# Optimization experiments

Hardware: AMD Instinct MI355X
Metric: run time of the kernel (lower is better)

Reference implementation:

```python
import jax, jax.numpy as jnp
import numpy as np
from jax import lax

B, T, I, H, O = 256, 128, 512, 1024, 512


def setup_inputs() -> dict:
    key = jax.random.key(0)
    ks = jax.random.split(key, 7)
    s = 1.0 / np.sqrt(H)  # PyTorch LSTM/Linear init bound
    x = jax.random.normal(ks[0], (B, T, I), dtype=jnp.float32)
    W_ih = jax.random.uniform(ks[1], (4 * H, I), jnp.float32, -s, s)
    W_hh = jax.random.uniform(ks[2], (4 * H, H), jnp.float32, -s, s)
    b_ih = jax.random.uniform(ks[3], (4 * H,), jnp.float32, -s, s)
    b_hh = jax.random.uniform(ks[4], (4 * H,), jnp.float32, -s, s)
    W_fc = jax.random.uniform(ks[5], (O, H), jnp.float32, -s, s)
    b_fc = jax.random.uniform(ks[6], (O,), jnp.float32, -s, s)
    return {"x": x, "W_ih": W_ih, "W_hh": W_hh, "b_ih": b_ih,
            "b_hh": b_hh, "W_fc": W_fc, "b_fc": b_fc}


def _lstm_last(x, W_ih, W_hh, b_ih, b_hh):
    # Precompute input contribution for all timesteps: [T, B, 4H]
    pre = jnp.einsum('bti,gi->tbg', x, W_ih) + b_ih + b_hh

    def step(carry, xg):
        h, c = carry
        gates = xg + h @ W_hh.T  # [B, 4H]
        i, f, g, o = jnp.split(gates, 4, axis=-1)  # PyTorch gate order i,f,g,o
        c = jax.nn.sigmoid(f) * c + jax.nn.sigmoid(i) * jnp.tanh(g)
        h = jax.nn.sigmoid(o) * jnp.tanh(c)
        return (h, c), None

    h0 = jnp.zeros((x.shape[0], W_hh.shape[1]), x.dtype)
    (h, c), _ = lax.scan(step, (h0, h0), pre)
    return h, c


def reference(x, W_ih, W_hh, b_ih, b_hh, W_fc, b_fc):
    h, c = _lstm_last(x, W_ih, W_hh, b_ih, b_hh)
    out = h @ W_fc.T + b_fc  # fc on last timestep hidden
    # hidden returned as (h_n, c_n) with leading n_layers=1 dim, as in PyTorch
    return out, (h[None], c[None])
```

## Files before the change

### kernel.cpp

```cpp
#include <hip/hip_runtime.h>

typedef short bf8 __attribute__((ext_vector_type(8)));
typedef float f32x4 __attribute__((ext_vector_type(4)));

static constexpr int BB = 256;
static constexpr int TT = 128;
static constexpr int II = 512;
static constexpr int HH = 1024;
static constexpr int OO = 512;
static constexpr int G4 = 4096;

static constexpr size_t OUT_H = (size_t)BB * OO;
static constexpr size_t OUT_C = OUT_H + (size_t)BB * HH;
static constexpr size_t HBUF  = (size_t)BB * HH;

__device__ __forceinline__ float bf2f(ushort u) {
    unsigned v = ((unsigned)u) << 16;
    return __builtin_bit_cast(float, v);
}
__device__ __forceinline__ ushort f2bf(float f) {
    unsigned x = __builtin_bit_cast(unsigned, f);
    x = x + 0x7FFFu + ((x >> 16) & 1u);
    return (ushort)(x >> 16);
}
__device__ __forceinline__ float sigf(float x) { return 1.0f / (1.0f + __expf(-x)); }
__device__ __forceinline__ float tanhf_(float x) { return 2.0f * sigf(2.0f * x) - 1.0f; }

__device__ __forceinline__ void st_wt_short(const ushort* p, uint v) {
    asm volatile("global_store_short %0, %1, off sc0 sc1" :: "v"(p), "v"(v) : "memory");
}
__device__ __forceinline__ void st_wt_b64(const ushort* p, uint2 v) {
    asm volatile("global_store_dwordx2 %0, %1, off sc0 sc1" :: "v"(p), "v"(v) : "memory");
}
__device__ __forceinline__ void ld_bp_ushort_issue(uint& dst, const ushort* p) {
    asm volatile("global_load_ushort %0, %1, off sc0 sc1" : "=v"(dst) : "v"(p) : "memory");
}
__device__ __forceinline__ void ld_bp_b128_issue(uint4& dst, const ushort* p) {
    asm volatile("global_load_dwordx4 %0, %1, off sc0 sc1" : "=v"(dst) : "v"(p) : "memory");
}
__device__ __forceinline__ void wait_vm0() {
    asm volatile("s_waitcnt vmcnt(0)" ::: "memory");
    __builtin_amdgcn_sched_barrier(0);
}

__device__ __forceinline__ void lightbar(int* slots, int bg, int gen) {
    asm volatile("s_waitcnt vmcnt(0) lgkmcnt(0)" ::: "memory");
    __builtin_amdgcn_sched_barrier(0);
    __syncthreads();
    int tid = threadIdx.x;
    if (tid == 0) {
        asm volatile("global_store_dword %0, %1, off sc0 sc1" :: "v"(slots + bg * 32), "v"(gen) : "memory");
    }
    if (tid < 64) {
        const int* sp = slots + tid * 32;
        int v;
        do {
            asm volatile("global_load_dword %0, %1, off sc0 sc1\n\ts_waitcnt vmcnt(0)"
                         : "=v"(v) : "v"(sp) : "memory");
            if (v >= gen) break;
            __builtin_amdgcn_s_sleep(1);
        } while (true);
    }
    __syncthreads();
}

__global__ void k_init(int* slots) {
    int i = blockIdx.x * 256 + threadIdx.x;
    if (i < 4 * 64 * 32) slots[i] = 0;
}

__global__ void k_cast(const float* __restrict__ src, ushort* __restrict__ dst, int n4) {
    int i = blockIdx.x * blockDim.x + threadIdx.x;
    int stride = gridDim.x * blockDim.x;
    for (; i < n4; i += stride) {
        float4 v = ((const float4*)src)[i];
        ushort4 o;
        o.x = f2bf(v.x); o.y = f2bf(v.y); o.z = f2bf(v.z); o.w = f2bf(v.w);
        ((ushort4*)dst)[i] = o;
    }
}

__global__ void k_prep_w(const float* __restrict__ w, ushort* __restrict__ wp,
                         const float* __restrict__ bi, const float* __restrict__ bh,
                         float* __restrict__ bp, int Kdim) {
    int p = blockIdx.x;
    int orig = ((p >> 4) & 3) * HH + ((p >> 6) << 4) + (p & 15);
    const float* src = w + (size_t)orig * Kdim;
    ushort* dst = wp + (size_t)p * Kdim;
    for (int k = threadIdx.x; k < Kdim; k += 256) dst[k] = f2bf(src[k]);
    if (threadIdx.x == 0 && bp) bp[p] = bi[orig] + bh[orig];
}

__global__ __launch_bounds__(256) void k_main(
    const float* __restrict__ x, const ushort* __restrict__ wpih,
    const float* __restrict__ bp, ushort* __restrict__ pre,
    const ushort* __restrict__ wphh, ushort* __restrict__ hbf,
    float* __restrict__ dout, int* slots_all, int SEG) {
    __shared__ ushort wl[32 * 2048];
    __shared__ ushort Al[64 * 32];
    __shared__ ushort Bl[128 * 32];

    int tid = threadIdx.x;
    int bid = blockIdx.x;
    int g  = bid >> 6;
    int bg = bid & 63;
    int j  = bg;
    int row0 = g << 6;
    int* slots = slots_all + g * 64 * 32;
    int gen = 0;

    {
        const ushort* wsrc = wphh + (size_t)(j << 6) * HH;
        for (int s = 0; s < 32; ++s) {
            int cidx = (s << 8) + tid;
            int c = cidx >> 7;
            int kc = cidx & 127;
            uint4 v = *(const uint4*)(wsrc + (size_t)c * HH + (kc << 3));
            int byte = ((kc >> 2) << 12) + ((((c << 6) + ((kc & 3) << 4))) ^ ((c & 7) << 4));
            *(uint4*)((char*)wl + byte) = v;
        }
        int r = tid >> 2, hc = (tid & 3) << 2;
        uint2 z; z.x = 0; z.y = 0;
        st_wt_b64(hbf + (size_t)(row0 + r) * HH + (j << 4) + hc, z);
    }

    int w = tid >> 6, l = tid & 63;
    int wm = w >> 1, wn = w & 1;
    int l15 = l & 15, kg = l >> 4;
    int swz = (l15 & 7) << 4;
    int wbase = ((l15 << 6) + (kg << 4)) ^ swz;

    int r0 = tid >> 2, kk = tid & 3;
    int sbyteA = ((r0 << 6) + (kk << 4)) ^ ((r0 & 7) << 4);
    int sbyteB1 = sbyteA + 4096;

    const ushort* hrow0 = hbf + (size_t)(row0 + (w << 4) + l15) * HH + (kg << 3);
    int drow = row0 + (w << 4) + (kg << 2);
    int hcol = (j << 4) + l15;
    ushort* hout0 = hbf + (size_t)drow * HH + hcol;
    const ushort* pbase = pre + (size_t)drow * G4 + (j << 6) + l15;
    float creg[4] = {0.f, 0.f, 0.f, 0.f};

    int nseg = TT / SEG;
    for (int sg = 0; sg < nseg; ++sg) {
        int t0 = sg * SEG;
        int ntiles = SEG << 5;
        for (int q = bg; q < ntiles; q += 64) {
            int trel = q >> 5;
            int t = t0 + trel;
            int n0 = (q & 31) << 7;
            const float* xa = x + ((size_t)(row0 + r0) * TT + t) * II + (kk << 3);
            const ushort* gb0 = wpih + (size_t)(n0 + r0) * II + (kk << 3);
            const ushort* gb1 = gb0 + (size_t)64 * II;
            f32x4 acc[2][4];
#pragma unroll
            for (int mi = 0; mi < 2; ++mi)
#pragma unroll
                for (int ni = 0; ni < 4; ++ni) acc[mi][ni] = f32x4{0.f, 0.f, 0.f, 0.f};
            float4 a0 = *(const float4*)xa;
            float4 a1 = *(const float4*)(xa + 4);
            uint4 b0v = *(const uint4*)gb0;
            uint4 b1v = *(const uint4*)gb1;
            for (int ko = 0; ko < 16; ++ko) {
                union { ushort us[8]; uint4 v; } pa;
                pa.us[0] = f2bf(a0.x); pa.us[1] = f2bf(a0.y); pa.us[2] = f2bf(a0.z); pa.us[3] = f2bf(a0.w);
                pa.us[4] = f2bf(a1.x); pa.us[5] = f2bf(a1.y); pa.us[6] = f2bf(a1.z); pa.us[7] = f2bf(a1.w);
                __syncthreads();
                *(uint4*)((char*)Al + sbyteA) = pa.v;
                *(uint4*)((char*)Bl + sbyteA) = b0v;
                *(uint4*)((char*)Bl + sbyteB1) = b1v;
                __syncthreads();
                if (ko < 15) {
                    int k = (ko + 1) << 5;
                    a0 = *(const float4*)(xa + k);
                    a1 = *(const float4*)(xa + k + 4);
                    b0v = *(const uint4*)(gb0 + k);
                    b1v = *(const uint4*)(gb1 + k);
                }
                bf8 af[2], bv[4];
#pragma unroll
                for (int mi = 0; mi < 2; ++mi)
                    af[mi] = *(const bf8*)((char*)Al + wm * 2048 + mi * 1024 + wbase);
#pragma unroll
                for (int ni = 0; ni < 4; ++ni)
                    bv[ni] = *(const bf8*)((char*)Bl + wn * 4096 + ni * 1024 + wbase);
#pragma unroll
                for (int mi = 0; mi < 2; ++mi)
#pragma unroll
                    for (int ni = 0; ni < 4; ++ni)
                        acc[mi][ni] = __builtin_amdgcn_mfma_f32_16x16x32_bf16(af[mi], bv[ni], acc[mi][ni], 0, 0, 0);
            }
#pragma unroll
            for (int ni = 0; ni < 4; ++ni) {
                int col = n0 + wn * 64 + ni * 16 + l15;
                float bias = bp[col];
#pragma unroll
                for (int mi = 0; mi < 2; ++mi) {
                    int arow = row0 + wm * 32 + mi * 16 + (kg << 2);
#pragma unroll
                    for (int r = 0; r < 4; ++r) {
                        const ushort* pp = pre + ((size_t)trel * BB + arow + r) * G4 + col;
                        st_wt_short(pp, (uint)f2bf(acc[mi][ni][r] + bias));
                    }
                }
            }
        }
        gen++; lightbar(slots, bg, gen);

        uint prn[16];
#pragma unroll
        for (int ni = 0; ni < 4; ++ni)
#pragma unroll
            for (int r = 0; r < 4; ++r)
                ld_bp_ushort_issue(prn[ni * 4 + r], pbase + (size_t)r * G4 + ni * 16);

        for (int trel = 0; trel < SEG; ++trel) {
            int t = t0 + trel;
            wait_vm0();
            f32x4 acc[4];
#pragma unroll
            for (int ni = 0; ni < 4; ++ni)
#pragma unroll
                for (int r = 0; r < 4; ++r) acc[ni][r] = bf2f((ushort)prn[ni * 4 + r]);

            const ushort* hr = hrow0 + (size_t)(t & 1) * HBUF;
#pragma unroll
            for (int c = 0; c < 4; ++c) {
                uint4 hv[8];
#pragma unroll
                for (int u = 0; u < 8; ++u)
                    ld_bp_b128_issue(hv[u], hr + ((c * 8 + u) << 5));
                wait_vm0();
#pragma unroll
                for (int u = 0; u < 8; ++u) {
                    int ko = c * 8 + u;
                    bf8 a = __builtin_bit_cast(bf8, hv[u]);
#pragma unroll
                    for (int ni = 0; ni < 4; ++ni) {
                        bf8 b = *(const bf8*)((char*)wl + ko * 4096 + ni * 1024 + wbase);
                        acc[ni] = __builtin_amdgcn_mfma_f32_16x16x32_bf16(a, b, acc[ni], 0, 0, 0);
                    }
                }
            }

            if (trel < SEG - 1) {
                const ushort* pn = pbase + (size_t)(trel + 1) * ((size_t)BB * G4);
#pragma unroll
                for (int ni = 0; ni < 4; ++ni)
#pragma unroll
                    for (int r = 0; r < 4; ++r)
                        ld_bp_ushort_issue(prn[ni * 4 + r], pn + (size_t)r * G4 + ni * 16);
            }

            ushort* ho = hout0 + (size_t)((t & 1) ^ 1) * HBUF;
            bool last = (t == TT - 1);
#pragma unroll
            for (int r = 0; r < 4; ++r) {
                float ig = sigf(acc[0][r]);
                float fg = sigf(acc[1][r]);
                float gg = tanhf_(acc[2][r]);
                float og = sigf(acc[3][r]);
                float c = fg * creg[r] + ig * gg;
                creg[r] = c;
                float h = og * tanhf_(c);
                st_wt_short(ho + (size_t)r * HH, (uint)f2bf(h));
                if (last) {
                    dout[OUT_H + (size_t)(drow + r) * HH + hcol] = h;
                    dout[OUT_C + (size_t)(drow + r) * HH + hcol] = c;
                }
            }
            gen++; lightbar(slots, bg, gen);
        }
    }
}

__global__ __launch_bounds__(256) void k_fc(const ushort* __restrict__ hbf,
                                            const ushort* __restrict__ wfc,
                                            const float* __restrict__ bfc,
                                            float* __restrict__ out) {
    int tid = threadIdx.x;
    int b0 = (blockIdx.x >> 3) << 6;
    int n0 = (blockIdx.x & 7) << 6;
    int w = tid >> 6, l = tid & 63;
    int l15 = l & 15, kg = l >> 4;
    const ushort* ha = hbf + (size_t)(b0 + (w << 4) + l15) * HH + (kg << 3);
    f32x4 acc[4];
#pragma unroll
    for (int ni = 0; ni < 4; ++ni) acc[ni] = f32x4{0.f, 0.f, 0.f, 0.f};
    for (int ko = 0; ko < 32; ++ko) {
        bf8 a = *(const bf8*)(ha + (ko << 5));
#pragma unroll
        for (int ni = 0; ni < 4; ++ni) {
            bf8 b = *(const bf8*)(wfc + (size_t)(n0 + ni * 16 + l15) * HH + (ko << 5) + (kg << 3));
            acc[ni] = __builtin_amdgcn_mfma_f32_16x16x32_bf16(a, b, acc[ni], 0, 0, 0);
        }
    }
    int drow = b0 + (w << 4) + (kg << 2);
#pragma unroll
    for (int ni = 0; ni < 4; ++ni) {
        int col = n0 + ni * 16 + l15;
        float bias = bfc[col];
#pragma unroll
        for (int r = 0; r < 4; ++r)
            out[(size_t)(drow + r) * OO + col] = acc[ni][r] + bias;
    }
}

extern "C" void kernel_launch(void* const* d_in, const int* in_sizes, int n_in,
                              void* d_out, int out_size, void* d_ws, size_t ws_size,
                              hipStream_t stream) {
    const float* x   = (const float*)d_in[0];
    const float* Wih = (const float*)d_in[1];
    const float* Whh = (const float*)d_in[2];
    const float* bih = (const float*)d_in[3];
    const float* bhh = (const float*)d_in[4];
    const float* Wfc = (const float*)d_in[5];
    const float* bfc = (const float*)d_in[6];
    float* out = (float*)d_out;

    char* ws = (char*)d_ws;
    size_t off = 0;
    ushort* wpih = (ushort*)(ws + off); off += (size_t)G4 * II * 2;
    ushort* wphh = (ushort*)(ws + off); off += (size_t)G4 * HH * 2;
    ushort* wfcb = (ushort*)(ws + off); off += (size_t)OO * HH * 2;
    float*  bp   = (float*)(ws + off);  off += (size_t)G4 * 4;
    ushort* hbf  = (ushort*)(ws + off); off += (size_t)2 * BB * HH * 2;
    int*    slots= (int*)(ws + off);    off += (size_t)4 * 64 * 32 * 4;
    size_t fixed = off;
    int SEG = 16;
    while (SEG > 1 && fixed + (size_t)SEG * BB * G4 * 2 > ws_size) SEG >>= 1;
    ushort* pre = (ushort*)(ws + off);

    k_init<<<32, 256, 0, stream>>>(slots);
    k_cast<<<256, 256, 0, stream>>>(Wfc, wfcb, OO * HH / 4);
    k_prep_w<<<G4, 256, 0, stream>>>(Wih, wpih, bih, bhh, bp, II);
    k_prep_w<<<G4, 256, 0, stream>>>(Whh, wphh, nullptr, nullptr, nullptr, HH);
    k_main<<<256, 256, 0, stream>>>(x, wpih, bp, pre, wphh, hbf, out, slots, SEG);
    k_fc<<<32, 256, 0, stream>>>(hbf, wfcb, bfc, out);
}
```

Before: 1.649 ms.

## Split LSTM kernel into producer and consumer blocks with a ring-buffered input projection

Splits the persistent kernel into 128 producer blocks, which compute the input projection into a two-slot ring of segment buffers, and 128 consumer blocks that run the recurrence. The two sides hand off through seg_done and seg_used counters. Each consumer now covers 128 batch rows (two M tiles per wave) and double-buffers its h loads with partial vmcnt waits. The aim is to overlap the input GEMM with the serial recurrence and remove the per-segment barrier across all blocks. The cost is that only half the blocks run the recurrence, so each does twice the MFMA work per step, and producer-to-consumer polling adds latency.

```diff
diff --git a/kernel.cpp b/kernel.cpp
--- a/kernel.cpp
+++ b/kernel.cpp
@@ -2,6 +2,7 @@
 
 typedef short bf8 __attribute__((ext_vector_type(8)));
 typedef float f32x4 __attribute__((ext_vector_type(4)));
+typedef uint u32x4 __attribute__((ext_vector_type(4)));
 
 static constexpr int BB = 256;
 static constexpr int TT = 128;
@@ -9,6 +10,9 @@
 static constexpr int HH = 1024;
 static constexpr int OO = 512;
 static constexpr int G4 = 4096;
+static constexpr int NCONS = 128;
+static constexpr int NPROD = 128;
+static constexpr int RING = 2;
 
 static constexpr size_t OUT_H = (size_t)BB * OO;
 static constexpr size_t OUT_C = OUT_H + (size_t)BB * HH;
@@ -29,18 +33,32 @@
 __device__ __forceinline__ void st_wt_short(const ushort* p, uint v) {
     asm volatile("global_store_short %0, %1, off sc0 sc1" :: "v"(p), "v"(v) : "memory");
 }
-__device__ __forceinline__ void st_wt_b64(const ushort* p, uint2 v) {
-    asm volatile("global_store_dwordx2 %0, %1, off sc0 sc1" :: "v"(p), "v"(v) : "memory");
+__device__ __forceinline__ void st_wt_b128(const ushort* p, u32x4 v) {
+    asm volatile("global_store_dwordx4 %0, %1, off sc0 sc1" :: "v"(p), "v"(v) : "memory");
 }
 __device__ __forceinline__ void ld_bp_ushort_issue(uint& dst, const ushort* p) {
     asm volatile("global_load_ushort %0, %1, off sc0 sc1" : "=v"(dst) : "v"(p) : "memory");
 }
-__device__ __forceinline__ void ld_bp_b128_issue(uint4& dst, const ushort* p) {
+__device__ __forceinline__ void ld_bp_b128_issue(u32x4& dst, const ushort* p) {
     asm volatile("global_load_dwordx4 %0, %1, off sc0 sc1" : "=v"(dst) : "v"(p) : "memory");
 }
 __device__ __forceinline__ void wait_vm0() {
     asm volatile("s_waitcnt vmcnt(0)" ::: "memory");
     __builtin_amdgcn_sched_barrier(0);
+}
+#define WAITVM(N) do { asm volatile("s_waitcnt vmcnt(" #N ")" ::: "memory"); \
+                       __builtin_amdgcn_sched_barrier(0); } while (0)
+
+template <int SLP>
+__device__ __forceinline__ int poll_ge(const int* p, int target) {
+    int v;
+    do {
+        asm volatile("global_load_dword %0, %1, off sc0 sc1\n\ts_waitcnt vmcnt(0)"
+                     : "=v"(v) : "v"(p) : "memory");
+        if (v >= target) break;
+        __builtin_amdgcn_s_sleep(SLP);
+    } while (true);
+    return v;
 }
 
 __device__ __forceinline__ void lightbar(int* slots, int bg, int gen) {
@@ -48,9 +66,8 @@
     __builtin_amdgcn_sched_barrier(0);
     __syncthreads();
     int tid = threadIdx.x;
-    if (tid == 0) {
+    if (tid == 0)
         asm volatile("global_store_dword %0, %1, off sc0 sc1" :: "v"(slots + bg * 32), "v"(gen) : "memory");
-    }
     if (tid < 64) {
         const int* sp = slots + tid * 32;
         int v;
@@ -64,9 +81,9 @@
     __syncthreads();
 }
 
-__global__ void k_init(int* slots) {
+__global__ void k_init(int* flags) {
     int i = blockIdx.x * 256 + threadIdx.x;
-    if (i < 4 * 64 * 32) slots[i] = 0;
+    if (i < 4608) flags[i] = 0;
 }
 
 __global__ void k_cast(const float* __restrict__ src, ushort* __restrict__ dst, int n4) {
@@ -95,18 +112,105 @@
     const float* __restrict__ x, const ushort* __restrict__ wpih,
     const float* __restrict__ bp, ushort* __restrict__ pre,
     const ushort* __restrict__ wphh, ushort* __restrict__ hbf,
-    float* __restrict__ dout, int* slots_all, int SEG) {
+    float* __restrict__ dout, int* flags, int SEG) {
     __shared__ ushort wl[32 * 2048];
     __shared__ ushort Al[64 * 32];
     __shared__ ushort Bl[128 * 32];
 
     int tid = threadIdx.x;
     int bid = blockIdx.x;
-    int g  = bid >> 6;
-    int bg = bid & 63;
-    int j  = bg;
-    int row0 = g << 6;
-    int* slots = slots_all + g * 64 * 32;
+    int* seg_done = flags + 4096;
+    int* seg_used = flags + 4224;
+    int nseg = TT / SEG;
+    size_t SEGEL = (size_t)SEG * BB * G4;
+
+    int w = tid >> 6, l = tid & 63;
+    int l15 = l & 15, kg = l >> 4;
+    int wbase = ((l15 << 6) + (kg << 4)) ^ ((l15 & 7) << 4);
+
+    if (bid >= NCONS) {
+        int pid = bid - NCONS;
+        int wm = w >> 1, wn = w & 1;
+        int r0 = tid >> 2, kk = tid & 3;
+        int sbyteA = ((r0 << 6) + (kk << 4)) ^ ((r0 & 7) << 4);
+        int sbyteB1 = sbyteA + 4096;
+        for (int sg = 0; sg < nseg; ++sg) {
+            if (sg >= RING) {
+                if (tid == 0) poll_ge<8>(seg_used + sg - RING, NCONS);
+                __syncthreads();
+            }
+            ushort* sb = pre + (size_t)(sg % RING) * SEGEL;
+            for (int i = 0; i < SEG; ++i) {
+                int q = pid + (i << 7);
+                int tm = q >> 5, tn = q & 31;
+                int trel = tm >> 2, b0 = (tm & 3) << 6, n0 = tn << 7;
+                int t = sg * SEG + trel;
+                const float* xa = x + ((size_t)(b0 + r0) * TT + t) * II + (kk << 3);
+                const ushort* gb0 = wpih + (size_t)(n0 + r0) * II + (kk << 3);
+                const ushort* gb1 = gb0 + (size_t)64 * II;
+                f32x4 acc[2][4];
+#pragma unroll
+                for (int mi = 0; mi < 2; ++mi)
+#pragma unroll
+                    for (int ni = 0; ni < 4; ++ni) acc[mi][ni] = f32x4{0.f, 0.f, 0.f, 0.f};
+                float4 a0 = *(const float4*)xa;
+                float4 a1 = *(const float4*)(xa + 4);
+                uint4 b0v = *(const uint4*)gb0;
+                uint4 b1v = *(const uint4*)gb1;
+                for (int ko = 0; ko < 16; ++ko) {
+                    union { ushort us[8]; uint4 v; } pa;
+                    pa.us[0] = f2bf(a0.x); pa.us[1] = f2bf(a0.y); pa.us[2] = f2bf(a0.z); pa.us[3] = f2bf(a0.w);
+                    pa.us[4] = f2bf(a1.x); pa.us[5] = f2bf(a1.y); pa.us[6] = f2bf(a1.z); pa.us[7] = f2bf(a1.w);
+                    __syncthreads();
+                    *(uint4*)((char*)Al + sbyteA) = pa.v;
+                    *(uint4*)((char*)Bl + sbyteA) = b0v;
+                    *(uint4*)((char*)Bl + sbyteB1) = b1v;
+                    __syncthreads();
+                    if (ko < 15) {
+                        int k = (ko + 1) << 5;
+                        a0 = *(const float4*)(xa + k);
+                        a1 = *(const float4*)(xa + k + 4);
+                        b0v = *(const uint4*)(gb0 + k);
+                        b1v = *(const uint4*)(gb1 + k);
+                    }
+                    bf8 af[2], bv[4];
+#pragma unroll
+                    for (int mi = 0; mi < 2; ++mi)
+                        af[mi] = *(const bf8*)((char*)Al + wm * 2048 + mi * 1024 + wbase);
+#pragma unroll
+                    for (int ni = 0; ni < 4; ++ni)
+                        bv[ni] = *(const bf8*)((char*)Bl + wn * 4096 + ni * 1024 + wbase);
+#pragma unroll
+                    for (int mi = 0; mi < 2; ++mi)
+#pragma unroll
+                        for (int ni = 0; ni < 4; ++ni)
+                            acc[mi][ni] = __builtin_amdgcn_mfma_f32_16x16x32_bf16(af[mi], bv[ni], acc[mi][ni], 0, 0, 0);
+                }
+#pragma unroll
+                for (int ni = 0; ni < 4; ++ni) {
+                    int col = n0 + wn * 64 + ni * 16 + l15;
+                    float bias = bp[col];
+#pragma unroll
+                    for (int mi = 0; mi < 2; ++mi) {
+                        int arow = b0 + wm * 32 + mi * 16 + (kg << 2);
+#pragma unroll
+                        for (int r = 0; r < 4; ++r)
+                            st_wt_short(sb + ((size_t)trel * BB + arow + r) * G4 + col,
+                                        (uint)f2bf(acc[mi][ni][r] + bias));
+                    }
+                }
+            }
+            asm volatile("s_waitcnt vmcnt(0)" ::: "memory");
+            __builtin_amdgcn_sched_barrier(0);
+            __syncthreads();
+            if (tid == 0) atomicAdd(seg_done + sg, 1);
+        }
+        return;
+    }
+
+    int g = bid >> 6, j = bid & 63;
+    int row0 = g << 7;
+    int* slots = flags + g * 2048;
     int gen = 0;
 
     {
@@ -119,157 +223,137 @@
             int byte = ((kc >> 2) << 12) + ((((c << 6) + ((kc & 3) << 4))) ^ ((c & 7) << 4));
             *(uint4*)((char*)wl + byte) = v;
         }
-        int r = tid >> 2, hc = (tid & 3) << 2;
-        uint2 z; z.x = 0; z.y = 0;
-        st_wt_b64(hbf + (size_t)(row0 + r) * HH + (j << 4) + hc, z);
-    }
-
-    int w = tid >> 6, l = tid & 63;
-    int wm = w >> 1, wn = w & 1;
-    int l15 = l & 15, kg = l >> 4;
-    int swz = (l15 & 7) << 4;
-    int wbase = ((l15 << 6) + (kg << 4)) ^ swz;
-
-    int r0 = tid >> 2, kk = tid & 3;
-    int sbyteA = ((r0 << 6) + (kk << 4)) ^ ((r0 & 7) << 4);
-    int sbyteB1 = sbyteA + 4096;
-
-    const ushort* hrow0 = hbf + (size_t)(row0 + (w << 4) + l15) * HH + (kg << 3);
-    int drow = row0 + (w << 4) + (kg << 2);
+        int r = tid >> 1, hc = (tid & 1) << 3;
+        u32x4 z = {0, 0, 0, 0};
+        st_wt_b128(hbf + (size_t)(row0 + r) * HH + (j << 4) + hc, z);
+    }
+
+    int rw = row0 + (w << 5);
+    const ushort* hA0 = hbf + (size_t)(rw + l15) * HH + (kg << 3);
+    const ushort* hA1 = hbf + (size_t)(rw + 16 + l15) * HH + (kg << 3);
+    int dr0 = rw + (kg << 2);
+    int dr1 = rw + 16 + (kg << 2);
     int hcol = (j << 4) + l15;
-    ushort* hout0 = hbf + (size_t)drow * HH + hcol;
-    const ushort* pbase = pre + (size_t)drow * G4 + (j << 6) + l15;
-    float creg[4] = {0.f, 0.f, 0.f, 0.f};
-
-    int nseg = TT / SEG;
+    ushort* ho0 = hbf + (size_t)dr0 * HH + hcol;
+    ushort* ho1 = hbf + (size_t)dr1 * HH + hcol;
+    float creg[8] = {0.f, 0.f, 0.f, 0.f, 0.f, 0.f, 0.f, 0.f};
+
+    gen++; lightbar(slots, j, gen);
+
+    uint prn[32];
     for (int sg = 0; sg < nseg; ++sg) {
-        int t0 = sg * SEG;
-        int ntiles = SEG << 5;
-        for (int q = bg; q < ntiles; q += 64) {
-            int trel = q >> 5;
-            int t = t0 + trel;
-            int n0 = (q & 31) << 7;
-            const float* xa = x + ((size_t)(row0 + r0) * TT + t) * II + (kk << 3);
-            const ushort* gb0 = wpih + (size_t)(n0 + r0) * II + (kk << 3);
-            const ushort* gb1 = gb0 + (size_t)64 * II;
-            f32x4 acc[2][4];
-#pragma unroll
-            for (int mi = 0; mi < 2; ++mi)
-#pragma unroll
-                for (int ni = 0; ni < 4; ++ni) acc[mi][ni] = f32x4{0.f, 0.f, 0.f, 0.f};
-            float4 a0 = *(const float4*)xa;
-            float4 a1 = *(const float4*)(xa + 4);
-            uint4 b0v = *(const uint4*)gb0;
-            uint4 b1v = *(const uint4*)gb1;
-            for (int ko = 0; ko < 16; ++ko) {
-                union { ushort us[8]; uint4 v; } pa;
-                pa.us[0] = f2bf(a0.x); pa.us[1] = f2bf(a0.y); pa.us[2] = f2bf(a0.z); pa.us[3] = f2bf(a0.w);
-                pa.us[4] = f2bf(a1.x); pa.us[5] = f2bf(a1.y); pa.us[6] = f2bf(a1.z); pa.us[7] = f2bf(a1.w);
-                __syncthreads();
-                *(uint4*)((char*)Al + sbyteA) = pa.v;
-                *(uint4*)((char*)Bl + sbyteA) = b0v;
-                *(uint4*)((char*)Bl + sbyteB1) = b1v;
-                __syncthreads();
-                if (ko < 15) {
-                    int k = (ko + 1) << 5;
-                    a0 = *(const float4*)(xa + k);
-                    a1 = *(const float4*)(xa + k + 4);
-                    b0v = *(const uint4*)(gb0 + k);
-                    b1v = *(const uint4*)(gb1 + k);
-                }
-                bf8 af[2], bv[4];
-#pragma unroll
-                for (int mi = 0; mi < 2; ++mi)
-                    af[mi] = *(const bf8*)((char*)Al + wm * 2048 + mi * 1024 + wbase);
+        ushort* sb = pre + (size_t)(sg % RING) * SEGEL;
+        if (sg > 0 && tid == 0) atomicAdd(seg_used + sg - 1, 1);
+        if (tid == 0) poll_ge<2>(seg_done + sg, NPROD);
+        __syncthreads();
+        {
+            const ushort* pn0 = sb + (size_t)dr0 * G4 + (j << 6) + l15;
+            const ushort* pn1 = sb + (size_t)dr1 * G4 + (j << 6) + l15;
+#pragma unroll
+            for (int ni = 0; ni < 4; ++ni)
+#pragma unroll
+                for (int r = 0; r < 4; ++r) {
+                    ld_bp_ushort_issue(prn[ni * 4 + r], pn0 + (size_t)r * G4 + (ni << 4));
+                    ld_bp_ushort_issue(prn[16 + ni * 4 + r], pn1 + (size_t)r * G4 + (ni << 4));
+                }
+            wait_vm0();
+        }
+
+        for (int trel = 0; trel < SEG; ++trel) {
+            int t = sg * SEG + trel;
+            const ushort* hr0 = hA0 + (size_t)(t & 1) * HBUF;
+            const ushort* hr1 = hA1 + (size_t)(t & 1) * HBUF;
+            u32x4 x0[8], x1[8], y0[8], y1[8];
+
+#define ISSUE8(B0, B1, C) \
+            _Pragma("unroll") \
+            for (int u = 0; u < 8; ++u) { \
+                ld_bp_b128_issue(B0[u], hr0 + (((C) * 8 + u) << 5)); \
+                ld_bp_b128_issue(B1[u], hr1 + (((C) * 8 + u) << 5)); \
+            }
+#define CONSUME8(B0, B1, C) \
+            _Pragma("unroll") \
+            for (int u = 0; u < 8; ++u) { \
+                int ko = (C) * 8 + u; \
+                bf8 a0 = __builtin_bit_cast(bf8, B0[u]); \
+                bf8 a1 = __builtin_bit_cast(bf8, B1[u]); \
+                _Pragma("unroll") \
+                for (int ni = 0; ni < 4; ++ni) { \
+                    bf8 b = *(const bf8*)((char*)wl + ko * 4096 + ni * 1024 + wbase); \
+                    acc0[ni] = __builtin_amdgcn_mfma_f32_16x16x32_bf16(a0, b, acc0[ni], 0, 0, 0); \
+                    acc1[ni] = __builtin_amdgcn_mfma_f32_16x16x32_bf16(a1, b, acc1[ni], 0, 0, 0); \
+                } \
+            }
+
+            f32x4 acc0[4], acc1[4];
+            ISSUE8(x0, x1, 0)
+            ISSUE8(y0, y1, 1)
+#pragma unroll
+            for (int ni = 0; ni < 4; ++ni)
+#pragma unroll
+                for (int r = 0; r < 4; ++r) {
+                    acc0[ni][r] = bf2f((ushort)prn[ni * 4 + r]);
+                    acc1[ni][r] = bf2f((ushort)prn[16 + ni * 4 + r]);
+                }
+            WAITVM(16);
+            CONSUME8(x0, x1, 0)
+            ISSUE8(x0, x1, 2)
+            WAITVM(16);
+            CONSUME8(y0, y1, 1)
+            ISSUE8(y0, y1, 3)
+            WAITVM(16);
+            CONSUME8(x0, x1, 2)
+            {
+                int nrel = (trel + 1 < SEG) ? trel + 1 : 0;
+                const ushort* pn0 = sb + ((size_t)nrel * BB + dr0) * G4 + (j << 6) + l15;
+                const ushort* pn1 = sb + ((size_t)nrel * BB + dr1) * G4 + (j << 6) + l15;
 #pragma unroll
                 for (int ni = 0; ni < 4; ++ni)
-                    bv[ni] = *(const bf8*)((char*)Bl + wn * 4096 + ni * 1024 + wbase);
-#pragma unroll
-                for (int mi = 0; mi < 2; ++mi)
-#pragma unroll
-                    for (int ni = 0; ni < 4; ++ni)
-                        acc[mi][ni] = __builtin_amdgcn_mfma_f32_16x16x32_bf16(af[mi], bv[ni], acc[mi][ni], 0, 0, 0);
-            }
-#pragma unroll
-            for (int ni = 0; ni < 4; ++ni) {
-                int col = n0 + wn * 64 + ni * 16 + l15;
-                float bias = bp[col];
-#pragma unroll
-                for (int mi = 0; mi < 2; ++mi) {
-                    int arow = row0 + wm * 32 + mi * 16 + (kg << 2);
 #pragma unroll
                     for (int r = 0; r < 4; ++r) {
-                        const ushort* pp = pre + ((size_t)trel * BB + arow + r) * G4 + col;
-                        st_wt_short(pp, (uint)f2bf(acc[mi][ni][r] + bias));
+                        ld_bp_ushort_issue(prn[ni * 4 + r], pn0 + (size_t)r * G4 + (ni << 4));
+                        ld_bp_ushort_issue(prn[16 + ni * 4 + r], pn1 + (size_t)r * G4 + (ni << 4));
                     }
-                }
-            }
-        }
-        gen++; lightbar(slots, bg, gen);
-
-        uint prn[16];
-#pragma unroll
-        for (int ni = 0; ni < 4; ++ni)
-#pragma unroll
-            for (int r = 0; r < 4; ++r)
-                ld_bp_ushort_issue(prn[ni * 4 + r], pbase + (size_t)r * G4 + ni * 16);
-
-        for (int trel = 0; trel < SEG; ++trel) {
-            int t = t0 + trel;
-            wait_vm0();
-            f32x4 acc[4];
-#pragma unroll
-            for (int ni = 0; ni < 4; ++ni)
-#pragma unroll
-                for (int r = 0; r < 4; ++r) acc[ni][r] = bf2f((ushort)prn[ni * 4 + r]);
-
-            const ushort* hr = hrow0 + (size_t)(t & 1) * HBUF;
-#pragma unroll
-            for (int c = 0; c < 4; ++c) {
-                uint4 hv[8];
-#pragma unroll
-                for (int u = 0; u < 8; ++u)
-                    ld_bp_b128_issue(hv[u], hr + ((c * 8 + u) << 5));
-                wait_vm0();
-#pragma unroll
-                for (int u = 0; u < 8; ++u) {
-                    int ko = c * 8 + u;
-                    bf8 a = __builtin_bit_cast(bf8, hv[u]);
-#pragma unroll
-                    for (int ni = 0; ni < 4; ++ni) {
-                        bf8 b = *(const bf8*)((char*)wl + ko * 4096 + ni * 1024 + wbase);
-                        acc[ni] = __builtin_amdgcn_mfma_f32_16x16x32_bf16(a, b, acc[ni], 0, 0, 0);
-                    }
-                }
-            }
-
-            if (trel < SEG - 1) {
-                const ushort* pn = pbase + (size_t)(trel + 1) * ((size_t)BB * G4);
-#pragma unroll
-                for (int ni = 0; ni < 4; ++ni)
-#pragma unroll
-                    for (int r = 0; r < 4; ++r)
-                        ld_bp_ushort_issue(prn[ni * 4 + r], pn + (size_t)r * G4 + ni * 16);
-            }
-
-            ushort* ho = hout0 + (size_t)((t & 1) ^ 1) * HBUF;
+            }
+            WAITVM(32);
+            CONSUME8(y0, y1, 3)
+#undef ISSUE8
+#undef CONSUME8
+
+            ushort* h0 = ho0 + (size_t)((t & 1) ^ 1) * HBUF;
+            ushort* h1 = ho1 + (size_t)((t & 1) ^ 1) * HBUF;
             bool last = (t == TT - 1);
 #pragma unroll
             for (int r = 0; r < 4; ++r) {
-                float ig = sigf(acc[0][r]);
-                float fg = sigf(acc[1][r]);
-                float gg = tanhf_(acc[2][r]);
-                float og = sigf(acc[3][r]);
+                float ig = sigf(acc0[0][r]);
+                float fg = sigf(acc0[1][r]);
+                float gg = tanhf_(acc0[2][r]);
+                float og = sigf(acc0[3][r]);
                 float c = fg * creg[r] + ig * gg;
                 creg[r] = c;
                 float h = og * tanhf_(c);
-                st_wt_short(ho + (size_t)r * HH, (uint)f2bf(h));
+                st_wt_short(h0 + (size_t)r * HH, (uint)f2bf(h));
                 if (last) {
-                    dout[OUT_H + (size_t)(drow + r) * HH + hcol] = h;
-                    dout[OUT_C + (size_t)(drow + r) * HH + hcol] = c;
-                }
-            }
-            gen++; lightbar(slots, bg, gen);
+                    dout[OUT_H + (size_t)(dr0 + r) * HH + hcol] = h;
+                    dout[OUT_C + (size_t)(dr0 + r) * HH + hcol] = c;
+                }
+            }
+#pragma unroll
+            for (int r = 0; r < 4; ++r) {
+                float ig = sigf(acc1[0][r]);
+                float fg = sigf(acc1[1][r]);
+                float gg = tanhf_(acc1[2][r]);
+                float og = sigf(acc1[3][r]);
+                float c = fg * creg[4 + r] + ig * gg;
+                creg[4 + r] = c;
+                float h = og * tanhf_(c);
+                st_wt_short(h1 + (size_t)r * HH, (uint)f2bf(h));
+                if (last) {
+                    dout[OUT_H + (size_t)(dr1 + r) * HH + hcol] = h;
+                    dout[OUT_C + (size_t)(dr1 + r) * HH + hcol] = c;
+                }
+            }
+            gen++; lightbar(slots, j, gen);
         }
     }
 }
@@ -325,16 +409,16 @@
     ushort* wfcb = (ushort*)(ws + off); off += (size_t)OO * HH * 2;
     float*  bp   = (float*)(ws + off);  off += (size_t)G4 * 4;
     ushort* hbf  = (ushort*)(ws + off); off += (size_t)2 * BB * HH * 2;
-    int*    slots= (int*)(ws + off);    off += (size_t)4 * 64 * 32 * 4;
+    int*    flags= (int*)(ws + off);    off += 4608 * 4;
     size_t fixed = off;
     int SEG = 16;
-    while (SEG > 1 && fixed + (size_t)SEG * BB * G4 * 2 > ws_size) SEG >>= 1;
+    while (SEG > 1 && fixed + (size_t)RING * SEG * BB * G4 * 2 > ws_size) SEG >>= 1;
     ushort* pre = (ushort*)(ws + off);
 
-    k_init<<<32, 256, 0, stream>>>(slots);
+    k_init<<<18, 256, 0, stream>>>(flags);
     k_cast<<<256, 256, 0, stream>>>(Wfc, wfcb, OO * HH / 4);
     k_prep_w<<<G4, 256, 0, stream>>>(Wih, wpih, bih, bhh, bp, II);
     k_prep_w<<<G4, 256, 0, stream>>>(Whh, wphh, nullptr, nullptr, nullptr, HH);
-    k_main<<<256, 256, 0, stream>>>(x, wpih, bp, pre, wphh, hbf, out, slots, SEG);
+    k_main<<<256, 256, 0, stream>>>(x, wpih, bp, pre, wphh, hbf, out, flags, SEG);
     k_fc<<<32, 256, 0, stream>>>(hbf, wfcb, bfc, out);
 }
```

After: 1.791 ms. 8.7% more time.

## Use per-timestep h buffers with cached loads and software-pipeline h fetches

Applied to the files above, without the earlier changes.

When the workspace allows, the hidden state is written to a separate buffer for each timestep (T+1 buffers) rather than a ping-pong pair. Because an address is never rewritten, the recurrent h loads can use ordinary cached global loads instead of cache-bypassing ones. The h-fetch loop is also double-buffered: two groups of 8 dwordx4 loads stay in flight with partial vmcnt waits, and the next step's preactivation loads are issued during compute instead of after it. The cost is a much larger workspace footprint, which can shrink SEG, and correctness now depends on cache coherence across blocks for never-reused addresses.

```diff
diff --git a/kernel.cpp b/kernel.cpp
--- a/kernel.cpp
+++ b/kernel.cpp
@@ -2,6 +2,7 @@
 
 typedef short bf8 __attribute__((ext_vector_type(8)));
 typedef float f32x4 __attribute__((ext_vector_type(4)));
+typedef uint u32x4 __attribute__((ext_vector_type(4)));
 
 static constexpr int BB = 256;
 static constexpr int TT = 128;
@@ -35,22 +36,26 @@
 __device__ __forceinline__ void ld_bp_ushort_issue(uint& dst, const ushort* p) {
     asm volatile("global_load_ushort %0, %1, off sc0 sc1" : "=v"(dst) : "v"(p) : "memory");
 }
-__device__ __forceinline__ void ld_bp_b128_issue(uint4& dst, const ushort* p) {
+__device__ __forceinline__ void ld_bp_b128_issue(u32x4& dst, const ushort* p) {
     asm volatile("global_load_dwordx4 %0, %1, off sc0 sc1" : "=v"(dst) : "v"(p) : "memory");
+}
+__device__ __forceinline__ void ld_c_b128_issue(u32x4& dst, const ushort* p) {
+    asm volatile("global_load_dwordx4 %0, %1, off" : "=v"(dst) : "v"(p) : "memory");
 }
 __device__ __forceinline__ void wait_vm0() {
     asm volatile("s_waitcnt vmcnt(0)" ::: "memory");
     __builtin_amdgcn_sched_barrier(0);
 }
+#define WAITVM(N) do { asm volatile("s_waitcnt vmcnt(" #N ")" ::: "memory"); \
+                       __builtin_amdgcn_sched_barrier(0); } while (0)
 
 __device__ __forceinline__ void lightbar(int* slots, int bg, int gen) {
     asm volatile("s_waitcnt vmcnt(0) lgkmcnt(0)" ::: "memory");
     __builtin_amdgcn_sched_barrier(0);
     __syncthreads();
     int tid = threadIdx.x;
-    if (tid == 0) {
+    if (tid == 0)
         asm volatile("global_store_dword %0, %1, off sc0 sc1" :: "v"(slots + bg * 32), "v"(gen) : "memory");
-    }
     if (tid < 64) {
         const int* sp = slots + tid * 32;
         int v;
@@ -64,9 +69,9 @@
     __syncthreads();
 }
 
-__global__ void k_init(int* slots) {
+__global__ void k_init(int* flags) {
     int i = blockIdx.x * 256 + threadIdx.x;
-    if (i < 4 * 64 * 32) slots[i] = 0;
+    if (i < 8192) flags[i] = 0;
 }
 
 __global__ void k_cast(const float* __restrict__ src, ushort* __restrict__ dst, int n4) {
@@ -91,23 +96,27 @@
     if (threadIdx.x == 0 && bp) bp[p] = bi[orig] + bh[orig];
 }
 
+template <int HMODE>
 __global__ __launch_bounds__(256) void k_main(
     const float* __restrict__ x, const ushort* __restrict__ wpih,
     const float* __restrict__ bp, ushort* __restrict__ pre,
     const ushort* __restrict__ wphh, ushort* __restrict__ hbf,
-    float* __restrict__ dout, int* slots_all, int SEG) {
+    float* __restrict__ dout, int* flags, int SEG) {
     __shared__ ushort wl[32 * 2048];
     __shared__ ushort Al[64 * 32];
     __shared__ ushort Bl[128 * 32];
 
     int tid = threadIdx.x;
     int bid = blockIdx.x;
-    int g  = bid >> 6;
-    int bg = bid & 63;
-    int j  = bg;
+    int g = bid >> 6, j = bid & 63;
     int row0 = g << 6;
-    int* slots = slots_all + g * 64 * 32;
+    int* slots = flags + g * 2048;
     int gen = 0;
+    int nseg = TT / SEG;
+
+    int w = tid >> 6, l = tid & 63;
+    int l15 = l & 15, kg = l >> 4;
+    int wbase = ((l15 << 6) + (kg << 4)) ^ ((l15 & 7) << 4);
 
     {
         const ushort* wsrc = wphh + (size_t)(j << 6) * HH;
@@ -124,28 +133,22 @@
         st_wt_b64(hbf + (size_t)(row0 + r) * HH + (j << 4) + hc, z);
     }
 
-    int w = tid >> 6, l = tid & 63;
     int wm = w >> 1, wn = w & 1;
-    int l15 = l & 15, kg = l >> 4;
-    int swz = (l15 & 7) << 4;
-    int wbase = ((l15 << 6) + (kg << 4)) ^ swz;
-
     int r0 = tid >> 2, kk = tid & 3;
     int sbyteA = ((r0 << 6) + (kk << 4)) ^ ((r0 & 7) << 4);
     int sbyteB1 = sbyteA + 4096;
 
-    const ushort* hrow0 = hbf + (size_t)(row0 + (w << 4) + l15) * HH + (kg << 3);
+    const ushort* hbase = hbf + (size_t)(row0 + (w << 4) + l15) * HH + (kg << 3);
     int drow = row0 + (w << 4) + (kg << 2);
     int hcol = (j << 4) + l15;
-    ushort* hout0 = hbf + (size_t)drow * HH + hcol;
+    ushort* hobase = hbf + (size_t)drow * HH + hcol;
     const ushort* pbase = pre + (size_t)drow * G4 + (j << 6) + l15;
     float creg[4] = {0.f, 0.f, 0.f, 0.f};
 
-    int nseg = TT / SEG;
     for (int sg = 0; sg < nseg; ++sg) {
         int t0 = sg * SEG;
         int ntiles = SEG << 5;
-        for (int q = bg; q < ntiles; q += 64) {
+        for (int q = j; q < ntiles; q += 64) {
             int trel = q >> 5;
             int t = t0 + trel;
             int n0 = (q & 31) << 7;
@@ -198,61 +201,77 @@
                 for (int mi = 0; mi < 2; ++mi) {
                     int arow = row0 + wm * 32 + mi * 16 + (kg << 2);
 #pragma unroll
-                    for (int r = 0; r < 4; ++r) {
-                        const ushort* pp = pre + ((size_t)trel * BB + arow + r) * G4 + col;
-                        st_wt_short(pp, (uint)f2bf(acc[mi][ni][r] + bias));
-                    }
+                    for (int r = 0; r < 4; ++r)
+                        st_wt_short(pre + ((size_t)trel * BB + arow + r) * G4 + col,
+                                    (uint)f2bf(acc[mi][ni][r] + bias));
                 }
             }
         }
-        gen++; lightbar(slots, bg, gen);
+        gen++; lightbar(slots, j, gen);
 
         uint prn[16];
 #pragma unroll
         for (int ni = 0; ni < 4; ++ni)
 #pragma unroll
             for (int r = 0; r < 4; ++r)
-                ld_bp_ushort_issue(prn[ni * 4 + r], pbase + (size_t)r * G4 + ni * 16);
+                ld_bp_ushort_issue(prn[ni * 4 + r], pbase + (size_t)r * G4 + (ni << 4));
+        wait_vm0();
 
         for (int trel = 0; trel < SEG; ++trel) {
             int t = t0 + trel;
-            wait_vm0();
+            int rb = HMODE ? (t & 1) : t;
+            int wb = HMODE ? ((t & 1) ^ 1) : (t + 1);
+            const ushort* hr = hbase + (size_t)rb * HBUF;
+            u32x4 xv[8], yv[8];
+
+#define ISSUE8(B, C) \
+            _Pragma("unroll") \
+            for (int u = 0; u < 8; ++u) { \
+                if constexpr (HMODE == 0) ld_c_b128_issue(B[u], hr + (((C) * 8 + u) << 5)); \
+                else ld_bp_b128_issue(B[u], hr + (((C) * 8 + u) << 5)); \
+            }
+#define CONSUME8(B, C) \
+            _Pragma("unroll") \
+            for (int u = 0; u < 8; ++u) { \
+                int ko = (C) * 8 + u; \
+                bf8 a = __builtin_bit_cast(bf8, B[u]); \
+                _Pragma("unroll") \
+                for (int ni = 0; ni < 4; ++ni) { \
+                    bf8 b = *(const bf8*)((char*)wl + ko * 4096 + ni * 1024 + wbase); \
+                    acc[ni] = __builtin_amdgcn_mfma_f32_16x16x32_bf16(a, b, acc[ni], 0, 0, 0); \
+                } \
+            }
+
             f32x4 acc[4];
+            ISSUE8(xv, 0)
+            ISSUE8(yv, 1)
 #pragma unroll
             for (int ni = 0; ni < 4; ++ni)
 #pragma unroll
                 for (int r = 0; r < 4; ++r) acc[ni][r] = bf2f((ushort)prn[ni * 4 + r]);
-
-            const ushort* hr = hrow0 + (size_t)(t & 1) * HBUF;
-#pragma unroll
-            for (int c = 0; c < 4; ++c) {
-                uint4 hv[8];
-#pragma unroll
-                for (int u = 0; u < 8; ++u)
-                    ld_bp_b128_issue(hv[u], hr + ((c * 8 + u) << 5));
-                wait_vm0();
-#pragma unroll
-                for (int u = 0; u < 8; ++u) {
-                    int ko = c * 8 + u;
-                    bf8 a = __builtin_bit_cast(bf8, hv[u]);
-#pragma unroll
-                    for (int ni = 0; ni < 4; ++ni) {
-                        bf8 b = *(const bf8*)((char*)wl + ko * 4096 + ni * 1024 + wbase);
-                        acc[ni] = __builtin_amdgcn_mfma_f32_16x16x32_bf16(a, b, acc[ni], 0, 0, 0);
-                    }
-                }
-            }
-
-            if (trel < SEG - 1) {
-                const ushort* pn = pbase + (size_t)(trel + 1) * ((size_t)BB * G4);
+            WAITVM(8);
+            CONSUME8(xv, 0)
+            ISSUE8(xv, 2)
+            WAITVM(8);
+            CONSUME8(yv, 1)
+            ISSUE8(yv, 3)
+            WAITVM(8);
+            CONSUME8(xv, 2)
+            {
+                int nrel = (trel + 1 < SEG) ? trel + 1 : 0;
+                const ushort* pnn = pre + ((size_t)nrel * BB + drow) * G4 + (j << 6) + l15;
 #pragma unroll
                 for (int ni = 0; ni < 4; ++ni)
 #pragma unroll
                     for (int r = 0; r < 4; ++r)
-                        ld_bp_ushort_issue(prn[ni * 4 + r], pn + (size_t)r * G4 + ni * 16);
-            }
-
-            ushort* ho = hout0 + (size_t)((t & 1) ^ 1) * HBUF;
+                        ld_bp_ushort_issue(prn[ni * 4 + r], pnn + (size_t)r * G4 + (ni << 4));
+            }
+            WAITVM(16);
+            CONSUME8(yv, 3)
+#undef ISSUE8
+#undef CONSUME8
+
+            ushort* ho = hobase + (size_t)wb * HBUF;
             bool last = (t == TT - 1);
 #pragma unroll
             for (int r = 0; r < 4; ++r) {
@@ -269,12 +288,12 @@
                     dout[OUT_C + (size_t)(drow + r) * HH + hcol] = c;
                 }
             }
-            gen++; lightbar(slots, bg, gen);
+            gen++; lightbar(slots, j, gen);
         }
     }
 }
 
-__global__ __launch_bounds__(256) void k_fc(const ushort* __restrict__ hbf,
+__global__ __launch_bounds__(256) void k_fc(const ushort* __restrict__ hlast,
                                             const ushort* __restrict__ wfc,
                                             const float* __restrict__ bfc,
                                             float* __restrict__ out) {
@@ -283,7 +302,7 @@
     int n0 = (blockIdx.x & 7) << 6;
     int w = tid >> 6, l = tid & 63;
     int l15 = l & 15, kg = l >> 4;
-    const ushort* ha = hbf + (size_t)(b0 + (w << 4) + l15) * HH + (kg << 3);
+    const ushort* ha = hlast + (size_t)(b0 + (w << 4) + l15) * HH + (kg << 3);
     f32x4 acc[4];
 #pragma unroll
     for (int ni = 0; ni < 4; ++ni) acc[ni] = f32x4{0.f, 0.f, 0.f, 0.f};
@@ -324,17 +343,28 @@
     ushort* wphh = (ushort*)(ws + off); off += (size_t)G4 * HH * 2;
     ushort* wfcb = (ushort*)(ws + off); off += (size_t)OO * HH * 2;
     float*  bp   = (float*)(ws + off);  off += (size_t)G4 * 4;
-    ushort* hbf  = (ushort*)(ws + off); off += (size_t)2 * BB * HH * 2;
-    int*    slots= (int*)(ws + off);    off += (size_t)4 * 64 * 32 * 4;
+    int*    flags= (int*)(ws + off);    off += 8192 * 4;
     size_t fixed = off;
-    int SEG = 16;
-    while (SEG > 1 && fixed + (size_t)SEG * BB * G4 * 2 > ws_size) SEG >>= 1;
-    ushort* pre = (ushort*)(ws + off);
-
-    k_init<<<32, 256, 0, stream>>>(slots);
+    size_t HB2 = (size_t)BB * HH * 2;
+
+    int HMODE = 0, SEG = 16;
+    size_t hsz = (size_t)(TT + 1) * HB2;
+    while (SEG > 1 && fixed + hsz + (size_t)SEG * BB * G4 * 2 > ws_size) SEG >>= 1;
+    if (fixed + hsz + (size_t)SEG * BB * G4 * 2 > ws_size) {
+        HMODE = 1; SEG = 16; hsz = 2 * HB2;
+        while (SEG > 1 && fixed + hsz + (size_t)SEG * BB * G4 * 2 > ws_size) SEG >>= 1;
+    }
+    ushort* hbf = (ushort*)(ws + fixed);
+    ushort* pre = (ushort*)(ws + fixed + hsz);
+    const ushort* hlast = HMODE ? hbf : (hbf + (size_t)TT * HBUF);
+
+    k_init<<<32, 256, 0, stream>>>(flags);
     k_cast<<<256, 256, 0, stream>>>(Wfc, wfcb, OO * HH / 4);
     k_prep_w<<<G4, 256, 0, stream>>>(Wih, wpih, bih, bhh, bp, II);
     k_prep_w<<<G4, 256, 0, stream>>>(Whh, wphh, nullptr, nullptr, nullptr, HH);
-    k_main<<<256, 256, 0, stream>>>(x, wpih, bp, pre, wphh, hbf, out, slots, SEG);
-    k_fc<<<32, 256, 0, stream>>>(hbf, wfcb, bfc, out);
-}
+    if (HMODE == 0)
+        k_main<0><<<256, 256, 0, stream>>>(x, wpih, bp, pre, wphh, hbf, out, flags, SEG);
+    else
+        k_main<1><<<256, 256, 0, stream>>>(x, wpih, bp, pre, wphh, hbf, out, flags, SEG);
+    k_fc<<<32, 256, 0, stream>>>(hlast, wfcb, bfc, out);
+}
```

Result: faster. 1.515 ms (-8.1%).
